# Optimization experiments

Measured on AMD Instinct MI355X. Metric: run time of the kernel, lower is better.

The kernel has to match this reference:

```python
import jax, jax.numpy as jnp
import numpy as np

N = 50000   # num_nodes
D = 128     # h_dim
R = 32      # num_rels * 2 (forward + inverse relations)
B = 8       # num_bases
E = 600000  # num_edges


def setup_inputs() -> dict:
    key = jax.random.key(0)
    ks = jax.random.split(key, 14)
    s = 1.0 / np.sqrt(D)
    return {
        "h_ids": jnp.arange(N, dtype=jnp.int32),
        "src": jax.random.randint(ks[0], (E,), 0, N),
        "dst": jax.random.randint(ks[1], (E,), 0, N),
        "etype": jax.random.randint(ks[2], (E,), 0, R),
        "norm": jax.random.uniform(ks[3], (E, 1), dtype=jnp.float32),
        "embedding": jax.random.normal(ks[4], (N, D), dtype=jnp.float32) * 0.05,
        "w_comp1": jax.random.normal(ks[5], (R, B), dtype=jnp.float32) * (1.0 / np.sqrt(B)),
        "bases1": jax.random.normal(ks[6], (B, D, D), dtype=jnp.float32) * s,
        "loop_w1": jax.random.normal(ks[7], (D, D), dtype=jnp.float32) * s,
        "bias1": jnp.zeros((D,), dtype=jnp.float32),
        "w_comp2": jax.random.normal(ks[8], (R, B), dtype=jnp.float32) * (1.0 / np.sqrt(B)),
        "bases2": jax.random.normal(ks[9], (B, D, D), dtype=jnp.float32) * s,
        "loop_w2": jax.random.normal(ks[10], (D, D), dtype=jnp.float32) * s,
        "bias2": jnp.zeros((D,), dtype=jnp.float32),
    }


def _rel_graph_conv(h, src, dst, etype, norm, w_comp, bases, loop_w, bias, act):
    # basis decomposition: W[r] = sum_b w_comp[r,b] * bases[b]
    W = jnp.einsum('rb,bio->rio', w_comp, bases)          # [R, D, D]
    # transform every node by every relation weight (dense GEMM)
    all_t = jnp.einsum('ni,rio->nro', h, W)               # [N, R, D]
    # per-edge gather of relation-specific transformed source features
    msg = all_t[src, etype] * norm                        # [E, D]
    # scatter-aggregate messages at destination nodes
    agg = jax.ops.segment_sum(msg, dst, num_segments=h.shape[0])  # [N, D]
    out = agg + h @ loop_w + bias                         # self-loop + bias
    return act(out) if act is not None else out


def reference(h_ids, src, dst, etype, norm, embedding,
              w_comp1, bases1, loop_w1, bias1,
              w_comp2, bases2, loop_w2, bias2):
    # EmbeddingLayer
    h = embedding[h_ids]                                  # [N, D]
    # hidden layer 0: relu activation (idx < num_hidden_layers-1)
    h = _rel_graph_conv(h, src, dst, etype, norm, w_comp1, bases1, loop_w1, bias1, jax.nn.relu)
    # hidden layer 1: no activation (last layer)
    h = _rel_graph_conv(h, src, dst, etype, norm, w_comp2, bases2, loop_w2, bias2, None)
    return h
```

## Files before the change

kernel.cpp:

```cpp
#include <hip/hip_runtime.h>

#define DD 128
#define NB 8
#define KTOT 1152

typedef unsigned int uint_t;
typedef __attribute__((ext_vector_type(8))) _Float16 half8v;
typedef __attribute__((ext_vector_type(2))) _Float16 half2v;
typedef __attribute__((ext_vector_type(4))) float f32x4;

static __device__ __forceinline__ void gld_lds16(const _Float16* g, _Float16* l)
{
  __builtin_amdgcn_global_load_lds(
      (const __attribute__((address_space(1))) void*)g,
      (__attribute__((address_space(3))) void*)l, 16, 0, 0);
}

static __device__ __forceinline__ half2v bc_h2(uint_t u)
{
  union { uint_t u; half2v h; } c; c.u = u; return c.h;
}

static __device__ __forceinline__ float fdot2(uint_t a, uint_t b, float acc)
{
#if __has_builtin(__builtin_amdgcn_fdot2)
  return __builtin_amdgcn_fdot2(bc_h2(a), bc_h2(b), acc, false);
#else
  half2v x = bc_h2(a), y = bc_h2(b);
  return acc + (float)x[0] * (float)y[0] + (float)x[1] * (float)y[1];
#endif
}

__global__ __launch_bounds__(256) void k_prep_w(
    const float* __restrict__ bases1, const float* __restrict__ loopw1,
    const float* __restrict__ bases2, const float* __restrict__ loopw2,
    _Float16* __restrict__ WcA)
{
  int i = blockIdx.x * 256 + threadIdx.x;
  if (i >= 2 * 36 * DD * 32) return;
  int layer = i / (36 * DD * 32);
  int rem   = i % (36 * DD * 32);
  int ks    = rem / (DD * 32);
  int rem2  = rem % (DD * 32);
  int feat  = rem2 / 32;
  int j     = rem2 % 32;
  int k     = ks * 32 + j;
  const float* basesL = layer ? bases2 : bases1;
  const float* loopwL = layer ? loopw2 : loopw1;
  float v;
  if (k < 1024) {
    int kk = k >> 3, b = k & 7;
    v = basesL[((size_t)b * DD + kk) * DD + feat];
  } else {
    v = loopwL[(size_t)(k - 1024) * DD + feat];
  }
  WcA[i] = (_Float16)v;
}

__global__ __launch_bounds__(256) void k_cast(
    const float* __restrict__ h, const int* __restrict__ ids,
    _Float16* __restrict__ hf, int N)
{
  int i = blockIdx.x * 256 + threadIdx.x;
  if (i >= N * (DD / 8)) return;
  int n  = i / (DD / 8);
  int k8 = (i % (DD / 8)) * 8;
  int row = ids ? ids[n] : n;
  const float* hp = h + (size_t)row * DD + k8;
  float4 v0 = *(const float4*)hp;
  float4 v1 = *(const float4*)(hp + 4);
  union { _Float16 e[8]; uint4 q; } p;
  p.e[0]=(_Float16)v0.x; p.e[1]=(_Float16)v0.y; p.e[2]=(_Float16)v0.z; p.e[3]=(_Float16)v0.w;
  p.e[4]=(_Float16)v1.x; p.e[5]=(_Float16)v1.y; p.e[6]=(_Float16)v1.z; p.e[7]=(_Float16)v1.w;
  *(uint4*)&hf[(size_t)n * DD + k8] = p.q;
}

__global__ __launch_bounds__(256) void k_zero(int* __restrict__ p, int n)
{
  int i = blockIdx.x * 256 + threadIdx.x;
  if (i < n) p[i] = 0;
}

__global__ __launch_bounds__(256) void k_hist(
    const int* __restrict__ dst, int* __restrict__ cnt,
    int* __restrict__ slotin, int E)
{
  int e = blockIdx.x * 256 + threadIdx.x;
  if (e < E) slotin[e] = atomicAdd(&cnt[dst[e]], 1);
}

__global__ __launch_bounds__(256) void k_bsum(
    const int* __restrict__ cnt, int* __restrict__ bsum, int N)
{
  __shared__ int s[256];
  int i = blockIdx.x * 256 + threadIdx.x;
  s[threadIdx.x] = (i < N) ? ((cnt[i] + 1) & ~1) : 0;
  __syncthreads();
  for (int off = 128; off > 0; off >>= 1) {
    if (threadIdx.x < off) s[threadIdx.x] += s[threadIdx.x + off];
    __syncthreads();
  }
  if (threadIdx.x == 0) bsum[blockIdx.x] = s[0];
}

__global__ __launch_bounds__(256) void k_scanb(
    const int* __restrict__ bsum, int* __restrict__ boff, int nb)
{
  __shared__ int s[256];
  int t = threadIdx.x;
  int own = (t < nb) ? bsum[t] : 0;
  s[t] = own;
  __syncthreads();
  for (int off = 1; off < 256; off <<= 1) {
    int v = (t >= off) ? s[t - off] : 0;
    __syncthreads();
    s[t] += v;
    __syncthreads();
  }
  if (t < nb) boff[t] = s[t] - own;
}

__global__ __launch_bounds__(256) void k_scan3(
    const int* __restrict__ cnt, const int* __restrict__ boff,
    int* __restrict__ row_start, int N)
{
  __shared__ int s[256];
  int t = threadIdx.x;
  int i = blockIdx.x * 256 + t;
  int c = (i < N) ? cnt[i] : 0;
  int v = (c + 1) & ~1;
  s[t] = v;
  __syncthreads();
  for (int off = 1; off < 256; off <<= 1) {
    int u = (t >= off) ? s[t - off] : 0;
    __syncthreads();
    s[t] += u;
    __syncthreads();
  }
  if (i < N) row_start[i] = boff[blockIdx.x] + s[t] - v;
}

__global__ __launch_bounds__(256) void k_place(
    const int* __restrict__ dst, const int* __restrict__ src,
    const int* __restrict__ etype, const float* __restrict__ norm,
    const int* __restrict__ row_start, const int* __restrict__ slotin,
    int4* __restrict__ en4, int E)
{
  int e = blockIdx.x * 256 + threadIdx.x;
  if (e < E) {
    int slot = row_start[dst[e]] + slotin[e];
    en4[slot] = make_int4(src[e], etype[e], __float_as_int(norm[e]), 0);
  }
}

__global__ __launch_bounds__(256) void k_payload_pair(
    const int4* __restrict__ en4,
    const float* __restrict__ wcomp1, const float* __restrict__ wcomp2,
    int* __restrict__ psrc,
    _Float16* __restrict__ c1, _Float16* __restrict__ c2, int npair)
{
  int i = blockIdx.x * 256 + threadIdx.x;
  if (i >= npair) return;
  int4 a = en4[2 * i], b = en4[2 * i + 1];
  float n0 = __int_as_float(a.z), n1 = __int_as_float(b.z);
  *(int2*)&psrc[2 * i] = make_int2(a.x, b.x);
  const float* w10 = wcomp1 + a.y * NB;
  const float* w11 = wcomp1 + b.y * NB;
  const float* w20 = wcomp2 + a.y * NB;
  const float* w21 = wcomp2 + b.y * NB;

  union { _Float16 h[16]; uint4 q[2]; } p;
  #pragma unroll
  for (int bb = 0; bb < NB; bb++) {
    p.h[bb * 2]     = (_Float16)(w10[bb] * n0);
    p.h[bb * 2 + 1] = (_Float16)(w11[bb] * n1);
  }
  *(uint4*)&c1[(size_t)i * 16]     = p.q[0];
  *(uint4*)&c1[(size_t)i * 16 + 8] = p.q[1];
  #pragma unroll
  for (int bb = 0; bb < NB; bb++) {
    p.h[bb * 2]     = (_Float16)(w20[bb] * n0);
    p.h[bb * 2 + 1] = (_Float16)(w21[bb] * n1);
  }
  *(uint4*)&c2[(size_t)i * 16]     = p.q[0];
  *(uint4*)&c2[(size_t)i * 16 + 8] = p.q[1];
}

__global__ __launch_bounds__(256) void k_agg(
    const int* __restrict__ rowst, const int* __restrict__ cnt,
    const int* __restrict__ psrc, const _Float16* __restrict__ cpair,
    const _Float16* __restrict__ hf,
    _Float16* __restrict__ agg, int N)
{
  int v = blockIdx.x * 4 + (threadIdx.x >> 6);
  if (v >= N) return;
  int lane = threadIdx.x & 63;
  const uint_t* hf32 = (const uint_t*)hf;
  const int beg = rowst[v];
  const int npairs = (cnt[v] + 1) >> 1;
  const uint_t* cp = (const uint_t*)cpair + (size_t)(beg >> 1) * 8;
  const int* ps = psrc + beg;

  float ax[NB] = {}, ay[NB] = {};
  int i = 0;
  for (; i + 4 <= npairs; i += 4) {
    uint_t u[8], lo[4], hi[4];
    #pragma unroll
    for (int q = 0; q < 8; q++)
      u[q] = hf32[(size_t)ps[2*i + q] * 64 + lane];
    #pragma unroll
    for (int q = 0; q < 4; q++) {
      lo[q] = __builtin_amdgcn_perm(u[2*q], u[2*q+1], 0x01000504);
      hi[q] = __builtin_amdgcn_perm(u[2*q], u[2*q+1], 0x03020706);
    }
    #pragma unroll
    for (int b = 0; b < NB; b++) {
      #pragma unroll
      for (int q = 0; q < 4; q++) {
        uint_t cc = cp[(size_t)(i + q) * 8 + b];
        ax[b] = fdot2(cc, lo[q], ax[b]);
        ay[b] = fdot2(cc, hi[q], ay[b]);
      }
    }
  }
  for (; i + 2 <= npairs; i += 2) {
    uint_t u0 = hf32[(size_t)ps[2*i + 0] * 64 + lane];
    uint_t u1 = hf32[(size_t)ps[2*i + 1] * 64 + lane];
    uint_t u2 = hf32[(size_t)ps[2*i + 2] * 64 + lane];
    uint_t u3 = hf32[(size_t)ps[2*i + 3] * 64 + lane];
    uint_t lo01 = __builtin_amdgcn_perm(u0, u1, 0x01000504);
    uint_t hi01 = __builtin_amdgcn_perm(u0, u1, 0x03020706);
    uint_t lo23 = __builtin_amdgcn_perm(u2, u3, 0x01000504);
    uint_t hi23 = __builtin_amdgcn_perm(u2, u3, 0x03020706);
    #pragma unroll
    for (int b = 0; b < NB; b++) {
      uint_t ca = cp[(size_t)i * 8 + b];
      uint_t cb = cp[(size_t)(i + 1) * 8 + b];
      ax[b] = fdot2(ca, lo01, ax[b]);
      ay[b] = fdot2(ca, hi01, ay[b]);
      ax[b] = fdot2(cb, lo23, ax[b]);
      ay[b] = fdot2(cb, hi23, ay[b]);
    }
  }
  if (i < npairs) {
    uint_t u0 = hf32[(size_t)ps[2*i + 0] * 64 + lane];
    uint_t u1 = hf32[(size_t)ps[2*i + 1] * 64 + lane];
    uint_t lo01 = __builtin_amdgcn_perm(u0, u1, 0x01000504);
    uint_t hi01 = __builtin_amdgcn_perm(u0, u1, 0x03020706);
    #pragma unroll
    for (int b = 0; b < NB; b++) {
      uint_t ca = cp[(size_t)i * 8 + b];
      ax[b] = fdot2(ca, lo01, ax[b]);
      ay[b] = fdot2(ca, hi01, ay[b]);
    }
  }

  union { _Float16 e[8]; uint4 q; } p0, p1;
  #pragma unroll
  for (int b = 0; b < NB; b++) { p0.e[b] = (_Float16)ax[b]; p1.e[b] = (_Float16)ay[b]; }
  uint4* dstp = (uint4*)&agg[(size_t)v * 1024 + lane * 16];
  dstp[0] = p0.q;
  dstp[1] = p1.q;
}

template <int LAYER>
__global__ __launch_bounds__(512) void k_mm(
    const _Float16* __restrict__ agg,
    const _Float16* __restrict__ hf,
    const _Float16* __restrict__ WcA,
    const float* __restrict__ bias,
    float* __restrict__ outf, _Float16* __restrict__ outh, int N)
{
  __shared__ _Float16 sB[2][4096];

  const int n0   = blockIdx.x * 64;
  const int wv   = threadIdx.x >> 6;
  const int lane = threadIdx.x & 63;
  const int l15  = lane & 15, l4 = lane >> 4;

  int nodeL = n0 + lane; if (nodeL >= N) nodeL = N - 1;

  f32x4 acc[4];
  #pragma unroll
  for (int b = 0; b < 4; b++) acc[b] = (f32x4)0.f;

  const int fbase = wv * 16 + l15;
  const int koff  = l4 * 8;

  auto STAGE = [&](int buf, int t) {
    const _Float16* g;
    if (t < 16) g = &agg[(size_t)nodeL * 1024 + t * 64 + wv * 8];
    else        g = &hf [(size_t)nodeL * DD   + (t - 16) * 64 + wv * 8];
    gld_lds16(g, &sB[buf][wv * 512]);
  };

  auto COMPUTE = [&](int buf, int t) {
    #pragma unroll
    for (int sub = 0; sub < 2; sub++) {
      const int ks = 2 * t + sub;
      half8v af = *(const half8v*)&WcA[((size_t)ks * DD + fbase) * 32 + koff];
      half8v bfr[4];
      #pragma unroll
      for (int nf = 0; nf < 4; nf++)
        bfr[nf] = *(const half8v*)&sB[buf][(sub * 4 + l4) * 512 + (nf * 16 + l15) * 8];
      #pragma unroll
      for (int nf = 0; nf < 4; nf++)
        acc[nf] = __builtin_amdgcn_mfma_f32_16x16x32_f16(af, bfr[nf], acc[nf], 0, 0, 0);
    }
  };

  STAGE(0, 0);
  __syncthreads();
  int cur = 0;
  for (int t = 0; t < 17; t++) {
    STAGE(cur ^ 1, t + 1);
    COMPUTE(cur, t);
    __syncthreads();
    cur ^= 1;
  }
  COMPUTE(cur, 17);

  #pragma unroll
  for (int nf = 0; nf < 4; nf++) {
    int n = n0 + nf * 16 + l15;
    if (n >= N) continue;
    int feat = wv * 16 + l4 * 4;
    if (LAYER == 1) {
      union { _Float16 e[4]; uint2 q; } p;
      #pragma unroll
      for (int r = 0; r < 4; r++)
        p.e[r] = (_Float16)fmaxf(acc[nf][r] + bias[feat + r], 0.f);
      *(uint2*)&outh[(size_t)n * DD + feat] = p.q;
    } else {
      float4 o;
      o.x = acc[nf][0] + bias[feat + 0];
      o.y = acc[nf][1] + bias[feat + 1];
      o.z = acc[nf][2] + bias[feat + 2];
      o.w = acc[nf][3] + bias[feat + 3];
      *(float4*)&outf[(size_t)n * DD + feat] = o;
    }
  }
}

extern "C" void kernel_launch(void* const* d_in, const int* in_sizes, int n_in,
                              void* d_out, int out_size, void* d_ws, size_t ws_size,
                              hipStream_t stream)
{
  const int*   h_ids     = (const int*)d_in[0];
  const int*   src       = (const int*)d_in[1];
  const int*   dst       = (const int*)d_in[2];
  const int*   etype     = (const int*)d_in[3];
  const float* norm      = (const float*)d_in[4];
  const float* embedding = (const float*)d_in[5];
  const float* w_comp1   = (const float*)d_in[6];
  const float* bases1    = (const float*)d_in[7];
  const float* loop_w1   = (const float*)d_in[8];
  const float* bias1     = (const float*)d_in[9];
  const float* w_comp2   = (const float*)d_in[10];
  const float* bases2    = (const float*)d_in[11];
  const float* loop_w2   = (const float*)d_in[12];
  const float* bias2     = (const float*)d_in[13];

  const int N = in_sizes[0];
  const int E = in_sizes[1];
  const int S = (E + N) & ~1;
  const int NPAIR = S >> 1;
  const int NBLK = (N + 255) / 256;

  char* base = (char*)d_ws;
  size_t off = 0;
  auto alloc = [&](size_t bytes) -> char* {
    char* p = base + off;
    off += (bytes + 255) & ~(size_t)255;
    return p;
  };
  _Float16* agg  = (_Float16*)alloc((size_t)N * 1024 * 2);
  _Float16* hfp  = (_Float16*)alloc((size_t)N * DD * 2);
  _Float16* h1h  = (_Float16*)alloc((size_t)N * DD * 2);
  _Float16* WcA  = (_Float16*)alloc((size_t)2 * 36 * DD * 32 * 2);
  int*      cnt    = (int*)   alloc((size_t)N * 4);
  int4*     en4    = (int4*)  alloc((size_t)S * 16);
  int*      rowst  = (int*)   alloc((size_t)N * 4);
  int*      bsum   = (int*)   alloc(256 * 4);
  int*      boff   = (int*)   alloc(256 * 4);
  int*      slotin = (int*)   alloc((size_t)E * 4);
  int*      psrc   = (int*)   alloc((size_t)S * 4);
  _Float16* c1     = (_Float16*)alloc((size_t)S * 8 * 2);
  _Float16* c2     = (_Float16*)alloc((size_t)S * 8 * 2);
  float*    out    = (float*)d_out;

  int zn = (int)(((char*)(en4 + S) - (char*)cnt) / 4);
  k_zero <<<(zn + 255) / 256, 256, 0, stream>>>(cnt, zn);
  k_hist <<<(E + 255) / 256, 256, 0, stream>>>(dst, cnt, slotin, E);
  k_bsum <<<NBLK, 256, 0, stream>>>(cnt, bsum, N);
  k_scanb<<<1, 256, 0, stream>>>(bsum, boff, NBLK);
  k_scan3<<<NBLK, 256, 0, stream>>>(cnt, boff, rowst, N);
  k_place<<<(E + 255) / 256, 256, 0, stream>>>(dst, src, etype, norm,
                                               rowst, slotin, en4, E);
  k_payload_pair<<<(NPAIR + 255) / 256, 256, 0, stream>>>(
      en4, w_comp1, w_comp2, psrc, c1, c2, NPAIR);

  k_prep_w<<<(2 * 36 * DD * 32 + 255) / 256, 256, 0, stream>>>(bases1, loop_w1, bases2, loop_w2, WcA);

  dim3 gmm((N + 63) / 64);
  int gagg = (N + 3) / 4;

  k_cast<<<(N * (DD / 8) + 255) / 256, 256, 0, stream>>>(embedding, h_ids, hfp, N);
  k_agg<<<gagg, 256, 0, stream>>>(rowst, cnt, psrc, c1, hfp, agg, N);
  k_mm<1><<<gmm, 512, 0, stream>>>(agg, hfp, WcA, bias1, nullptr, h1h, N);

  k_agg<<<gagg, 256, 0, stream>>>(rowst, cnt, psrc, c2, h1h, agg, N);
  k_mm<2><<<gmm, 512, 0, stream>>>(agg, h1h, WcA + (size_t)36 * DD * 32, bias2, out, nullptr, N);
}
```

Baseline: 244.7 us.

## Fuse edge aggregation into per-layer GEMM kernel and shrink zero-init

Merges the per-node basis aggregation kernel into the matrix-multiply kernel. Each 512-thread block now aggregates its own 64 nodes into the agg buffer, then runs the GEMM after a block barrier, cutting two launches and keeping the agg rows likely hot in cache. The large zero-fill of the workspace is replaced by zeroing only the counters, with padding slots written in the scan and a total count used to bound payload processing. The risk is lower aggregation parallelism per block (8 nodes per wave serially) and a possibly weaker GEMM pipeline because the gather phase runs before it.

```diff
diff --git a/kernel.cpp b/kernel.cpp
--- a/kernel.cpp
+++ b/kernel.cpp
@@ -104,7 +104,8 @@
 }
 
 __global__ __launch_bounds__(256) void k_scanb(
-    const int* __restrict__ bsum, int* __restrict__ boff, int nb)
+    const int* __restrict__ bsum, int* __restrict__ boff,
+    int* __restrict__ tot, int nb)
 {
   __shared__ int s[256];
   int t = threadIdx.x;
@@ -118,11 +119,12 @@
     __syncthreads();
   }
   if (t < nb) boff[t] = s[t] - own;
+  if (t == nb - 1) tot[0] = s[t];
 }
 
 __global__ __launch_bounds__(256) void k_scan3(
     const int* __restrict__ cnt, const int* __restrict__ boff,
-    int* __restrict__ row_start, int N)
+    int* __restrict__ row_start, int4* __restrict__ en4, int N)
 {
   __shared__ int s[256];
   int t = threadIdx.x;
@@ -137,7 +139,11 @@
     s[t] += u;
     __syncthreads();
   }
-  if (i < N) row_start[i] = boff[blockIdx.x] + s[t] - v;
+  if (i < N) {
+    int rs = boff[blockIdx.x] + s[t] - v;
+    row_start[i] = rs;
+    if (c & 1) en4[rs + c] = make_int4(0, 0, 0, 0);
+  }
 }
 
 __global__ __launch_bounds__(256) void k_place(
@@ -154,13 +160,13 @@
 }
 
 __global__ __launch_bounds__(256) void k_payload_pair(
-    const int4* __restrict__ en4,
+    const int4* __restrict__ en4, const int* __restrict__ tot,
     const float* __restrict__ wcomp1, const float* __restrict__ wcomp2,
     int* __restrict__ psrc,
     _Float16* __restrict__ c1, _Float16* __restrict__ c2, int npair)
 {
   int i = blockIdx.x * 256 + threadIdx.x;
-  if (i >= npair) return;
+  if (i >= npair || 2 * i >= tot[0]) return;
   int4 a = en4[2 * i], b = en4[2 * i + 1];
   float n0 = __int_as_float(a.z), n1 = __int_as_float(b.z);
   *(int2*)&psrc[2 * i] = make_int2(a.x, b.x);
@@ -186,89 +192,14 @@
   *(uint4*)&c2[(size_t)i * 16 + 8] = p.q[1];
 }
 
-__global__ __launch_bounds__(256) void k_agg(
+template <int LAYER>
+__global__ __launch_bounds__(512) void k_layer(
     const int* __restrict__ rowst, const int* __restrict__ cnt,
     const int* __restrict__ psrc, const _Float16* __restrict__ cpair,
     const _Float16* __restrict__ hf,
-    _Float16* __restrict__ agg, int N)
-{
-  int v = blockIdx.x * 4 + (threadIdx.x >> 6);
-  if (v >= N) return;
-  int lane = threadIdx.x & 63;
-  const uint_t* hf32 = (const uint_t*)hf;
-  const int beg = rowst[v];
-  const int npairs = (cnt[v] + 1) >> 1;
-  const uint_t* cp = (const uint_t*)cpair + (size_t)(beg >> 1) * 8;
-  const int* ps = psrc + beg;
-
-  float ax[NB] = {}, ay[NB] = {};
-  int i = 0;
-  for (; i + 4 <= npairs; i += 4) {
-    uint_t u[8], lo[4], hi[4];
-    #pragma unroll
-    for (int q = 0; q < 8; q++)
-      u[q] = hf32[(size_t)ps[2*i + q] * 64 + lane];
-    #pragma unroll
-    for (int q = 0; q < 4; q++) {
-      lo[q] = __builtin_amdgcn_perm(u[2*q], u[2*q+1], 0x01000504);
-      hi[q] = __builtin_amdgcn_perm(u[2*q], u[2*q+1], 0x03020706);
-    }
-    #pragma unroll
-    for (int b = 0; b < NB; b++) {
-      #pragma unroll
-      for (int q = 0; q < 4; q++) {
-        uint_t cc = cp[(size_t)(i + q) * 8 + b];
-        ax[b] = fdot2(cc, lo[q], ax[b]);
-        ay[b] = fdot2(cc, hi[q], ay[b]);
-      }
-    }
-  }
-  for (; i + 2 <= npairs; i += 2) {
-    uint_t u0 = hf32[(size_t)ps[2*i + 0] * 64 + lane];
-    uint_t u1 = hf32[(size_t)ps[2*i + 1] * 64 + lane];
-    uint_t u2 = hf32[(size_t)ps[2*i + 2] * 64 + lane];
-    uint_t u3 = hf32[(size_t)ps[2*i + 3] * 64 + lane];
-    uint_t lo01 = __builtin_amdgcn_perm(u0, u1, 0x01000504);
-    uint_t hi01 = __builtin_amdgcn_perm(u0, u1, 0x03020706);
-    uint_t lo23 = __builtin_amdgcn_perm(u2, u3, 0x01000504);
-    uint_t hi23 = __builtin_amdgcn_perm(u2, u3, 0x03020706);
-    #pragma unroll
-    for (int b = 0; b < NB; b++) {
-      uint_t ca = cp[(size_t)i * 8 + b];
-      uint_t cb = cp[(size_t)(i + 1) * 8 + b];
-      ax[b] = fdot2(ca, lo01, ax[b]);
-      ay[b] = fdot2(ca, hi01, ay[b]);
-      ax[b] = fdot2(cb, lo23, ax[b]);
-      ay[b] = fdot2(cb, hi23, ay[b]);
-    }
-  }
-  if (i < npairs) {
-    uint_t u0 = hf32[(size_t)ps[2*i + 0] * 64 + lane];
-    uint_t u1 = hf32[(size_t)ps[2*i + 1] * 64 + lane];
-    uint_t lo01 = __builtin_amdgcn_perm(u0, u1, 0x01000504);
-    uint_t hi01 = __builtin_amdgcn_perm(u0, u1, 0x03020706);
-    #pragma unroll
-    for (int b = 0; b < NB; b++) {
-      uint_t ca = cp[(size_t)i * 8 + b];
-      ax[b] = fdot2(ca, lo01, ax[b]);
-      ay[b] = fdot2(ca, hi01, ay[b]);
-    }
-  }
-
-  union { _Float16 e[8]; uint4 q; } p0, p1;
-  #pragma unroll
-  for (int b = 0; b < NB; b++) { p0.e[b] = (_Float16)ax[b]; p1.e[b] = (_Float16)ay[b]; }
-  uint4* dstp = (uint4*)&agg[(size_t)v * 1024 + lane * 16];
-  dstp[0] = p0.q;
-  dstp[1] = p1.q;
-}
-
-template <int LAYER>
-__global__ __launch_bounds__(512) void k_mm(
-    const _Float16* __restrict__ agg,
-    const _Float16* __restrict__ hf,
     const _Float16* __restrict__ WcA,
     const float* __restrict__ bias,
+    _Float16* __restrict__ agg,
     float* __restrict__ outf, _Float16* __restrict__ outh, int N)
 {
   __shared__ _Float16 sB[2][4096];
@@ -277,6 +208,79 @@
   const int wv   = threadIdx.x >> 6;
   const int lane = threadIdx.x & 63;
   const int l15  = lane & 15, l4 = lane >> 4;
+  const uint_t* hf32 = (const uint_t*)hf;
+
+  for (int r = 0; r < 8; r++) {
+    int v = n0 + wv * 8 + r;
+    if (v >= N) break;
+    const int beg = rowst[v];
+    const int npairs = (cnt[v] + 1) >> 1;
+    const uint_t* cp = (const uint_t*)cpair + (size_t)(beg >> 1) * 8;
+    const int* ps = psrc + beg;
+
+    float ax[NB] = {}, ay[NB] = {};
+    int i = 0;
+    for (; i + 4 <= npairs; i += 4) {
+      uint_t u[8], lo[4], hi[4];
+      #pragma unroll
+      for (int q = 0; q < 8; q++)
+        u[q] = hf32[(size_t)ps[2*i + q] * 64 + lane];
+      #pragma unroll
+      for (int q = 0; q < 4; q++) {
+        lo[q] = __builtin_amdgcn_perm(u[2*q], u[2*q+1], 0x01000504);
+        hi[q] = __builtin_amdgcn_perm(u[2*q], u[2*q+1], 0x03020706);
+      }
+      #pragma unroll
+      for (int b = 0; b < NB; b++) {
+        #pragma unroll
+        for (int q = 0; q < 4; q++) {
+          uint_t cc = cp[(size_t)(i + q) * 8 + b];
+          ax[b] = fdot2(cc, lo[q], ax[b]);
+          ay[b] = fdot2(cc, hi[q], ay[b]);
+        }
+      }
+    }
+    for (; i + 2 <= npairs; i += 2) {
+      uint_t u0 = hf32[(size_t)ps[2*i + 0] * 64 + lane];
+      uint_t u1 = hf32[(size_t)ps[2*i + 1] * 64 + lane];
+      uint_t u2 = hf32[(size_t)ps[2*i + 2] * 64 + lane];
+      uint_t u3 = hf32[(size_t)ps[2*i + 3] * 64 + lane];
+      uint_t lo01 = __builtin_amdgcn_perm(u0, u1, 0x01000504);
+      uint_t hi01 = __builtin_amdgcn_perm(u0, u1, 0x03020706);
+      uint_t lo23 = __builtin_amdgcn_perm(u2, u3, 0x01000504);
+      uint_t hi23 = __builtin_amdgcn_perm(u2, u3, 0x03020706);
+      #pragma unroll
+      for (int b = 0; b < NB; b++) {
+        uint_t ca = cp[(size_t)i * 8 + b];
+        uint_t cb = cp[(size_t)(i + 1) * 8 + b];
+        ax[b] = fdot2(ca, lo01, ax[b]);
+        ay[b] = fdot2(ca, hi01, ay[b]);
+        ax[b] = fdot2(cb, lo23, ax[b]);
+        ay[b] = fdot2(cb, hi23, ay[b]);
+      }
+    }
+    if (i < npairs) {
+      uint_t u0 = hf32[(size_t)ps[2*i + 0] * 64 + lane];
+      uint_t u1 = hf32[(size_t)ps[2*i + 1] * 64 + lane];
+      uint_t lo01 = __builtin_amdgcn_perm(u0, u1, 0x01000504);
+      uint_t hi01 = __builtin_amdgcn_perm(u0, u1, 0x03020706);
+      #pragma unroll
+      for (int b = 0; b < NB; b++) {
+        uint_t ca = cp[(size_t)i * 8 + b];
+        ax[b] = fdot2(ca, lo01, ax[b]);
+        ay[b] = fdot2(ca, hi01, ay[b]);
+      }
+    }
+
+    union { _Float16 e[8]; uint4 q; } p0, p1;
+    #pragma unroll
+    for (int b = 0; b < NB; b++) { p0.e[b] = (_Float16)ax[b]; p1.e[b] = (_Float16)ay[b]; }
+    uint4* dstp = (uint4*)&agg[(size_t)v * 1024 + lane * 16];
+    dstp[0] = p0.q;
+    dstp[1] = p1.q;
+  }
+
+  __syncthreads();
 
   int nodeL = n0 + lane; if (nodeL >= N) nodeL = N - 1;
 
@@ -383,32 +387,31 @@
   int*      rowst  = (int*)   alloc((size_t)N * 4);
   int*      bsum   = (int*)   alloc(256 * 4);
   int*      boff   = (int*)   alloc(256 * 4);
+  int*      tot    = (int*)   alloc(256);
   int*      slotin = (int*)   alloc((size_t)E * 4);
   int*      psrc   = (int*)   alloc((size_t)S * 4);
   _Float16* c1     = (_Float16*)alloc((size_t)S * 8 * 2);
   _Float16* c2     = (_Float16*)alloc((size_t)S * 8 * 2);
   float*    out    = (float*)d_out;
 
-  int zn = (int)(((char*)(en4 + S) - (char*)cnt) / 4);
-  k_zero <<<(zn + 255) / 256, 256, 0, stream>>>(cnt, zn);
+  k_zero <<<(N + 255) / 256, 256, 0, stream>>>(cnt, N);
   k_hist <<<(E + 255) / 256, 256, 0, stream>>>(dst, cnt, slotin, E);
   k_bsum <<<NBLK, 256, 0, stream>>>(cnt, bsum, N);
-  k_scanb<<<1, 256, 0, stream>>>(bsum, boff, NBLK);
-  k_scan3<<<NBLK, 256, 0, stream>>>(cnt, boff, rowst, N);
+  k_scanb<<<1, 256, 0, stream>>>(bsum, boff, tot, NBLK);
+  k_scan3<<<NBLK, 256, 0, stream>>>(cnt, boff, rowst, en4, N);
   k_place<<<(E + 255) / 256, 256, 0, stream>>>(dst, src, etype, norm,
                                                rowst, slotin, en4, E);
   k_payload_pair<<<(NPAIR + 255) / 256, 256, 0, stream>>>(
-      en4, w_comp1, w_comp2, psrc, c1, c2, NPAIR);
+      en4, tot, w_comp1, w_comp2, psrc, c1, c2, NPAIR);
 
   k_prep_w<<<(2 * 36 * DD * 32 + 255) / 256, 256, 0, stream>>>(bases1, loop_w1, bases2, loop_w2, WcA);
 
-  dim3 gmm((N + 63) / 64);
-  int gagg = (N + 3) / 4;
+  dim3 gl((N + 63) / 64);
 
   k_cast<<<(N * (DD / 8) + 255) / 256, 256, 0, stream>>>(embedding, h_ids, hfp, N);
-  k_agg<<<gagg, 256, 0, stream>>>(rowst, cnt, psrc, c1, hfp, agg, N);
-  k_mm<1><<<gmm, 512, 0, stream>>>(agg, hfp, WcA, bias1, nullptr, h1h, N);
-
-  k_agg<<<gagg, 256, 0, stream>>>(rowst, cnt, psrc, c2, h1h, agg, N);
-  k_mm<2><<<gmm, 512, 0, stream>>>(agg, h1h, WcA + (size_t)36 * DD * 32, bias2, out, nullptr, N);
-}
+  k_layer<1><<<gl, 512, 0, stream>>>(rowst, cnt, psrc, c1, hfp, WcA, bias1,
+                                     agg, nullptr, h1h, N);
+  k_layer<2><<<gl, 512, 0, stream>>>(rowst, cnt, psrc, c2, h1h,
+                                     WcA + (size_t)36 * DD * 32, bias2,
+                                     agg, out, nullptr, N);
+}
```

Result: slower. 263.7 us (+7.8%).

## Zero only padding slots, skip unused pairs, vectorize aggregation loads

Applied to the files above, without the earlier changes.

The full zeroing of the count and edge-slot buffers is replaced by zeroing only the count array, with padding slots of odd-degree nodes zeroed explicitly in the scan kernel. A total-slot count from the block scan lets the payload kernel skip pairs beyond the used range. The aggregation kernel now loads source indices as int2 and coefficient payloads as uint4 vectors, and its tail loops are simplified to a single-pair loop. The aim is less memset traffic and fewer, wider loads, at the cost of relying on every used slot being written or explicitly zeroed.

```diff
diff --git a/kernel.cpp b/kernel.cpp
--- a/kernel.cpp
+++ b/kernel.cpp
@@ -104,7 +104,8 @@
 }
 
 __global__ __launch_bounds__(256) void k_scanb(
-    const int* __restrict__ bsum, int* __restrict__ boff, int nb)
+    const int* __restrict__ bsum, int* __restrict__ boff,
+    int* __restrict__ tot, int nb)
 {
   __shared__ int s[256];
   int t = threadIdx.x;
@@ -118,11 +119,12 @@
     __syncthreads();
   }
   if (t < nb) boff[t] = s[t] - own;
+  if (t == nb - 1) tot[0] = s[t];
 }
 
 __global__ __launch_bounds__(256) void k_scan3(
     const int* __restrict__ cnt, const int* __restrict__ boff,
-    int* __restrict__ row_start, int N)
+    int* __restrict__ row_start, int4* __restrict__ en4, int N)
 {
   __shared__ int s[256];
   int t = threadIdx.x;
@@ -137,7 +139,11 @@
     s[t] += u;
     __syncthreads();
   }
-  if (i < N) row_start[i] = boff[blockIdx.x] + s[t] - v;
+  if (i < N) {
+    int rs = boff[blockIdx.x] + s[t] - v;
+    row_start[i] = rs;
+    if (c & 1) en4[rs + c] = make_int4(0, 0, 0, 0);
+  }
 }
 
 __global__ __launch_bounds__(256) void k_place(
@@ -154,13 +160,13 @@
 }
 
 __global__ __launch_bounds__(256) void k_payload_pair(
-    const int4* __restrict__ en4,
+    const int4* __restrict__ en4, const int* __restrict__ tot,
     const float* __restrict__ wcomp1, const float* __restrict__ wcomp2,
     int* __restrict__ psrc,
     _Float16* __restrict__ c1, _Float16* __restrict__ c2, int npair)
 {
   int i = blockIdx.x * 256 + threadIdx.x;
-  if (i >= npair) return;
+  if (i >= npair || 2 * i >= tot[0]) return;
   int4 a = en4[2 * i], b = en4[2 * i + 1];
   float n0 = __int_as_float(a.z), n1 = __int_as_float(b.z);
   *(int2*)&psrc[2 * i] = make_int2(a.x, b.x);
@@ -198,60 +204,59 @@
   const uint_t* hf32 = (const uint_t*)hf;
   const int beg = rowst[v];
   const int npairs = (cnt[v] + 1) >> 1;
-  const uint_t* cp = (const uint_t*)cpair + (size_t)(beg >> 1) * 8;
+  const uint4* cp4 = (const uint4*)cpair + (size_t)(beg >> 1) * 2;
   const int* ps = psrc + beg;
 
+  union U8 { uint4 q[2]; uint_t c[8]; };
   float ax[NB] = {}, ay[NB] = {};
   int i = 0;
   for (; i + 4 <= npairs; i += 4) {
-    uint_t u[8], lo[4], hi[4];
-    #pragma unroll
-    for (int q = 0; q < 8; q++)
-      u[q] = hf32[(size_t)ps[2*i + q] * 64 + lane];
-    #pragma unroll
-    for (int q = 0; q < 4; q++) {
-      lo[q] = __builtin_amdgcn_perm(u[2*q], u[2*q+1], 0x01000504);
-      hi[q] = __builtin_amdgcn_perm(u[2*q], u[2*q+1], 0x03020706);
-    }
+    int2 s01 = *(const int2*)(ps + 2*i);
+    int2 s23 = *(const int2*)(ps + 2*i + 2);
+    int2 s45 = *(const int2*)(ps + 2*i + 4);
+    int2 s67 = *(const int2*)(ps + 2*i + 6);
+    uint_t u0 = hf32[(size_t)s01.x * 64 + lane];
+    uint_t u1 = hf32[(size_t)s01.y * 64 + lane];
+    uint_t u2 = hf32[(size_t)s23.x * 64 + lane];
+    uint_t u3 = hf32[(size_t)s23.y * 64 + lane];
+    uint_t u4 = hf32[(size_t)s45.x * 64 + lane];
+    uint_t u5 = hf32[(size_t)s45.y * 64 + lane];
+    uint_t u6 = hf32[(size_t)s67.x * 64 + lane];
+    uint_t u7 = hf32[(size_t)s67.y * 64 + lane];
+    uint_t lo[4], hi[4];
+    lo[0] = __builtin_amdgcn_perm(u0, u1, 0x01000504);
+    hi[0] = __builtin_amdgcn_perm(u0, u1, 0x03020706);
+    lo[1] = __builtin_amdgcn_perm(u2, u3, 0x01000504);
+    hi[1] = __builtin_amdgcn_perm(u2, u3, 0x03020706);
+    lo[2] = __builtin_amdgcn_perm(u4, u5, 0x01000504);
+    hi[2] = __builtin_amdgcn_perm(u4, u5, 0x03020706);
+    lo[3] = __builtin_amdgcn_perm(u6, u7, 0x01000504);
+    hi[3] = __builtin_amdgcn_perm(u6, u7, 0x03020706);
+    U8 C0, C1, C2, C3;
+    C0.q[0] = cp4[2*i + 0]; C0.q[1] = cp4[2*i + 1];
+    C1.q[0] = cp4[2*i + 2]; C1.q[1] = cp4[2*i + 3];
+    C2.q[0] = cp4[2*i + 4]; C2.q[1] = cp4[2*i + 5];
+    C3.q[0] = cp4[2*i + 6]; C3.q[1] = cp4[2*i + 7];
     #pragma unroll
     for (int b = 0; b < NB; b++) {
-      #pragma unroll
-      for (int q = 0; q < 4; q++) {
-        uint_t cc = cp[(size_t)(i + q) * 8 + b];
-        ax[b] = fdot2(cc, lo[q], ax[b]);
-        ay[b] = fdot2(cc, hi[q], ay[b]);
-      }
+      ax[b] = fdot2(C0.c[b], lo[0], ax[b]); ay[b] = fdot2(C0.c[b], hi[0], ay[b]);
+      ax[b] = fdot2(C1.c[b], lo[1], ax[b]); ay[b] = fdot2(C1.c[b], hi[1], ay[b]);
+      ax[b] = fdot2(C2.c[b], lo[2], ax[b]); ay[b] = fdot2(C2.c[b], hi[2], ay[b]);
+      ax[b] = fdot2(C3.c[b], lo[3], ax[b]); ay[b] = fdot2(C3.c[b], hi[3], ay[b]);
     }
   }
-  for (; i + 2 <= npairs; i += 2) {
-    uint_t u0 = hf32[(size_t)ps[2*i + 0] * 64 + lane];
-    uint_t u1 = hf32[(size_t)ps[2*i + 1] * 64 + lane];
-    uint_t u2 = hf32[(size_t)ps[2*i + 2] * 64 + lane];
-    uint_t u3 = hf32[(size_t)ps[2*i + 3] * 64 + lane];
-    uint_t lo01 = __builtin_amdgcn_perm(u0, u1, 0x01000504);
-    uint_t hi01 = __builtin_amdgcn_perm(u0, u1, 0x03020706);
-    uint_t lo23 = __builtin_amdgcn_perm(u2, u3, 0x01000504);
-    uint_t hi23 = __builtin_amdgcn_perm(u2, u3, 0x03020706);
+  for (; i < npairs; i++) {
+    int2 s01 = *(const int2*)(ps + 2*i);
+    uint_t u0 = hf32[(size_t)s01.x * 64 + lane];
+    uint_t u1 = hf32[(size_t)s01.y * 64 + lane];
+    uint_t lo0 = __builtin_amdgcn_perm(u0, u1, 0x01000504);
+    uint_t hi0 = __builtin_amdgcn_perm(u0, u1, 0x03020706);
+    U8 C0;
+    C0.q[0] = cp4[2*i + 0]; C0.q[1] = cp4[2*i + 1];
     #pragma unroll
     for (int b = 0; b < NB; b++) {
-      uint_t ca = cp[(size_t)i * 8 + b];
-      uint_t cb = cp[(size_t)(i + 1) * 8 + b];
-      ax[b] = fdot2(ca, lo01, ax[b]);
-      ay[b] = fdot2(ca, hi01, ay[b]);
-      ax[b] = fdot2(cb, lo23, ax[b]);
-      ay[b] = fdot2(cb, hi23, ay[b]);
-    }
-  }
-  if (i < npairs) {
-    uint_t u0 = hf32[(size_t)ps[2*i + 0] * 64 + lane];
-    uint_t u1 = hf32[(size_t)ps[2*i + 1] * 64 + lane];
-    uint_t lo01 = __builtin_amdgcn_perm(u0, u1, 0x01000504);
-    uint_t hi01 = __builtin_amdgcn_perm(u0, u1, 0x03020706);
-    #pragma unroll
-    for (int b = 0; b < NB; b++) {
-      uint_t ca = cp[(size_t)i * 8 + b];
-      ax[b] = fdot2(ca, lo01, ax[b]);
-      ay[b] = fdot2(ca, hi01, ay[b]);
+      ax[b] = fdot2(C0.c[b], lo0, ax[b]);
+      ay[b] = fdot2(C0.c[b], hi0, ay[b]);
     }
   }
 
@@ -383,22 +388,22 @@
   int*      rowst  = (int*)   alloc((size_t)N * 4);
   int*      bsum   = (int*)   alloc(256 * 4);
   int*      boff   = (int*)   alloc(256 * 4);
+  int*      tot    = (int*)   alloc(256);
   int*      slotin = (int*)   alloc((size_t)E * 4);
   int*      psrc   = (int*)   alloc((size_t)S * 4);
   _Float16* c1     = (_Float16*)alloc((size_t)S * 8 * 2);
   _Float16* c2     = (_Float16*)alloc((size_t)S * 8 * 2);
   float*    out    = (float*)d_out;
 
-  int zn = (int)(((char*)(en4 + S) - (char*)cnt) / 4);
-  k_zero <<<(zn + 255) / 256, 256, 0, stream>>>(cnt, zn);
+  k_zero <<<(N + 255) / 256, 256, 0, stream>>>(cnt, N);
   k_hist <<<(E + 255) / 256, 256, 0, stream>>>(dst, cnt, slotin, E);
   k_bsum <<<NBLK, 256, 0, stream>>>(cnt, bsum, N);
-  k_scanb<<<1, 256, 0, stream>>>(bsum, boff, NBLK);
-  k_scan3<<<NBLK, 256, 0, stream>>>(cnt, boff, rowst, N);
+  k_scanb<<<1, 256, 0, stream>>>(bsum, boff, tot, NBLK);
+  k_scan3<<<NBLK, 256, 0, stream>>>(cnt, boff, rowst, en4, N);
   k_place<<<(E + 255) / 256, 256, 0, stream>>>(dst, src, etype, norm,
                                                rowst, slotin, en4, E);
   k_payload_pair<<<(NPAIR + 255) / 256, 256, 0, stream>>>(
-      en4, w_comp1, w_comp2, psrc, c1, c2, NPAIR);
+      en4, tot, w_comp1, w_comp2, psrc, c1, c2, NPAIR);
 
   k_prep_w<<<(2 * 36 * DD * 32 + 255) / 256, 256, 0, stream>>>(bases1, loop_w1, bases2, loop_w2, WcA);
 
```

Measured after the change: 252.3 us. 3.1% more time.
